# Kernel tuning notes

Hardware: AMD Instinct MI355X
Metric: run time of the kernel (lower is better)

The kernel has to match this reference:

```python
import jax, jax.numpy as jnp
import numpy as np

D_MODEL = 1024
N_HEADS = 16
HEAD_DIM = D_MODEL // N_HEADS


def setup_inputs() -> dict:
    key = jax.random.key(0)
    k0, k1, k2, k3, k4, k5 = jax.random.split(key, 6)
    s = 1.0 / np.sqrt(D_MODEL)
    return {
        "q": jax.random.normal(k0, (2, 2048, D_MODEL), dtype=jnp.float32),
        "Wq": jax.random.normal(k1, (D_MODEL, D_MODEL), dtype=jnp.float32) * s,
        "Wk": jax.random.normal(k2, (D_MODEL, D_MODEL), dtype=jnp.float32) * s,
        "Wv": jax.random.normal(k3, (D_MODEL, D_MODEL), dtype=jnp.float32) * s,
        "Wo": jax.random.normal(k4, (D_MODEL, D_MODEL), dtype=jnp.float32) * s,
        "bo": jax.random.normal(k5, (D_MODEL,), dtype=jnp.float32) * 0.01,
    }


def _split_heads(x):
    b, s, _ = x.shape
    return x.reshape(b, s, N_HEADS, HEAD_DIM).transpose(0, 2, 1, 3)  # [b,h,s,d]


def reference(q, Wq, Wk, Wv, Wo, bo):
    # self-attention: k = v = q
    qh = _split_heads(q @ Wq)  # [b,h,s,d]
    kh = _split_heads(q @ Wk)
    vh = _split_heads(q @ Wv)
    scale = 1.0 / np.sqrt(HEAD_DIM).astype(np.float32)
    scores = jnp.einsum("bhqd,bhkd->bhqk", qh, kh) * scale
    attn = jax.nn.softmax(scores, axis=-1)
    ctx = jnp.einsum("bhqk,bhkd->bhqd", attn, vh)
    b, h, s, d = ctx.shape
    ctx = ctx.transpose(0, 2, 1, 3).reshape(b, s, h * d)
    return ctx @ Wo + bo
```

## Files before the change

kernel.cpp:

```cpp
#include <hip/hip_runtime.h>
#include <cstdint>

typedef unsigned short u16;
typedef __bf16 bf16x8 __attribute__((ext_vector_type(8)));
typedef __bf16 bf16x2 __attribute__((ext_vector_type(2)));
typedef float floatx4 __attribute__((ext_vector_type(4)));
typedef unsigned short u16x4 __attribute__((ext_vector_type(4)));
typedef unsigned short u16x8 __attribute__((ext_vector_type(8)));

#define MFMA16(a, b, c) __builtin_amdgcn_mfma_f32_16x16x32_bf16((a), (b), (c), 0, 0, 0)
#define QSCALE_LOG2E 0.18033688011112042f


typedef __attribute__((address_space(3))) void as3_void;
typedef __attribute__((address_space(1))) void as1_void;

static __device__ __forceinline__ void async_load16(const void* g, void* l) {
  __builtin_amdgcn_global_load_lds((as1_void*)(uintptr_t)g, (as3_void*)(uintptr_t)l,
                                   16, 0, 0);
}

static __device__ __forceinline__ u16 f2bf(float f) {
  union { float f; unsigned int u; } v; v.f = f;
  unsigned int u = v.u;
  u += 0x7fffu + ((u >> 16) & 1u);
  return (u16)(u >> 16);
}

static __device__ __forceinline__ u16x4 pack_bf4(float a, float b, float c, float d) {
#if __has_builtin(__builtin_amdgcn_cvt_pk_bf16_f32)
  union { u16x4 v4; bf16x2 v2[2]; } u;
  u.v2[0] = __builtin_amdgcn_cvt_pk_bf16_f32(a, b);
  u.v2[1] = __builtin_amdgcn_cvt_pk_bf16_f32(c, d);
  return u.v4;
#else
  u16x4 r; r[0] = f2bf(a); r[1] = f2bf(b); r[2] = f2bf(c); r[3] = f2bf(d);
  return r;
#endif
}

static __device__ __forceinline__ unsigned pack_bf2(float a, float b) {
#if __has_builtin(__builtin_amdgcn_cvt_pk_bf16_f32)
  union { bf16x2 v; unsigned u; } x;
  x.v = __builtin_amdgcn_cvt_pk_bf16_f32(a, b);
  return x.u;
#else
  return (unsigned)f2bf(a) | ((unsigned)f2bf(b) << 16);
#endif
}

static __device__ __forceinline__ float fast_exp2(float x) {
#if __has_builtin(__builtin_amdgcn_exp2f)
  return __builtin_amdgcn_exp2f(x);
#else
  return exp2f(x);
#endif
}


__global__ __launch_bounds__(256) void prep_kernel(
    const float* __restrict__ w0, const float* __restrict__ w1,
    const float* __restrict__ w2, const float* __restrict__ w3,
    u16* __restrict__ wout,
    const float* __restrict__ xin, u16* __restrict__ xout) {
  if (blockIdx.z == 4) {
    int blk = blockIdx.y * 16 + blockIdx.x;
    size_t base = (size_t)blk * 16384 + (size_t)threadIdx.x * 8;
#pragma unroll
    for (int r = 0; r < 8; r++) {
      size_t i = base + (size_t)r * 2048;
      float4 a = *(const float4*)(xin + i);
      float4 b = *(const float4*)(xin + i + 4);
      u16x8 o;
      o[0] = f2bf(a.x); o[1] = f2bf(a.y); o[2] = f2bf(a.z); o[3] = f2bf(a.w);
      o[4] = f2bf(b.x); o[5] = f2bf(b.y); o[6] = f2bf(b.z); o[7] = f2bf(b.w);
      *(u16x8*)(xout + i) = o;
    }
    return;
  }
  __shared__ u16 t[64][65];
  const float* in = (blockIdx.z == 0) ? w0 : (blockIdx.z == 1) ? w1
                    : (blockIdx.z == 2) ? w2 : w3;
  u16* oz = wout + (size_t)blockIdx.z * (1024 * 1024);
  const int tid = threadIdx.x;
  const int x = tid & 63, y0 = tid >> 6;
  const int bx = blockIdx.x * 64, by = blockIdx.y * 64;
#pragma unroll
  for (int p = 0; p < 16; p++) {
    int y = y0 + p * 4;
    t[y][x] = f2bf(in[(size_t)(by + y) * 1024 + bx + x]);
  }
  __syncthreads();
#pragma unroll
  for (int p = 0; p < 16; p++) {
    int r = y0 + p * 4;
    oz[(size_t)(bx + r) * 1024 + by + x] = t[x][r];
  }
}


__global__ __launch_bounds__(256, 3) void gemm_qkv_kernel(
    const u16* __restrict__ A, const u16* __restrict__ BT,
    u16* __restrict__ out, u16* __restrict__ outVT) {
  __shared__ u16 As[128 * 32];
  __shared__ u16 Bs[128 * 32];
  __shared__ u16 tb[64 * 136];
  const int tid = threadIdx.x;
  const int w = tid >> 6, lane = tid & 63;
  const int bm = blockIdx.y * 128, bn = blockIdx.x * 128;
  const int z = blockIdx.z;
  const int K = 1024, N = 1024;
  const u16* Bz = BT + (size_t)z * N * K;

  const int c0 = w * 2, c1 = c0 + 1;
  const int mA0 = c0 * 16 + (lane >> 2), mA1 = c1 * 16 + (lane >> 2);
  const int kg0 = (lane & 3) ^ ((mA0 >> 1) & 3);
  const int kg1 = (lane & 3) ^ ((mA1 >> 1) & 3);
  const u16* agp0 = A + (size_t)(bm + mA0) * K + kg0 * 8;
  const u16* agp1 = A + (size_t)(bm + mA1) * K + kg1 * 8;
  const u16* bgp0 = Bz + (size_t)(bn + mA0) * K + kg0 * 8;
  const u16* bgp1 = Bz + (size_t)(bn + mA1) * K + kg1 * 8;
  u16* ald0 = As + c0 * 512; u16* ald1 = As + c1 * 512;
  u16* bld0 = Bs + c0 * 512; u16* bld1 = Bs + c1 * 512;

  const int wm = (w >> 1) * 64, wn = (w & 1) * 64;
  floatx4 acc[4][4] = {};

  int a_off[4], b_off[4];
#pragma unroll
  for (int i = 0; i < 4; i++) {
    int m = wm + i * 16 + (lane & 15);
    a_off[i] = m * 32 + (((lane >> 4) ^ ((m >> 1) & 3)) * 8);
    int n = wn + i * 16 + (lane & 15);
    b_off[i] = n * 32 + (((lane >> 4) ^ ((n >> 1) & 3)) * 8);
  }

  for (int k0 = 0; k0 < K; k0 += 32) {
    __syncthreads();
    async_load16(agp0 + k0, ald0);
    async_load16(agp1 + k0, ald1);
    async_load16(bgp0 + k0, bld0);
    async_load16(bgp1 + k0, bld1);
    __syncthreads();
    bf16x8 af[4], bf[4];
#pragma unroll
    for (int i = 0; i < 4; i++) af[i] = *(const bf16x8*)(As + a_off[i]);
#pragma unroll
    for (int j = 0; j < 4; j++) bf[j] = *(const bf16x8*)(Bs + b_off[j]);
#pragma unroll
    for (int i = 0; i < 4; i++)
#pragma unroll
      for (int j = 0; j < 4; j++)
        acc[i][j] = MFMA16(af[i], bf[j], acc[i][j]);
  }

  const int roff = (lane >> 4) * 4;
  const int coff = lane & 15;
  if (z == 2) {
    const int b = bm >> 11, s0 = bm & 2047;
#pragma unroll
    for (int half = 0; half < 2; half++) {
      __syncthreads();
      if ((w & 1) == half) {
#pragma unroll
        for (int i = 0; i < 4; i++) {
          int s_local = wm + i * 16 + roff;
#pragma unroll
          for (int j = 0; j < 4; j++) {
            int c_local = j * 16 + coff;
            u16x4 pk = pack_bf4(acc[i][j][0], acc[i][j][1],
                                acc[i][j][2], acc[i][j][3]);
            *(u16x4*)(tb + c_local * 136 + s_local) = pk;
          }
        }
      }
      __syncthreads();
#pragma unroll
      for (int p = 0; p < 4; p++) {
        int c_local = (tid >> 4) & 15;
        int row = p * 16 + c_local;
        int so = tid & 15;
        int cg = bn + half * 64 + row;
        int h = cg >> 6, d = cg & 63;
        u16x8 vv = *(const u16x8*)(tb + row * 136 + so * 8);
        *(u16x8*)(outVT + ((size_t)(b * 16 + h) * 64 + d) * 2048 + s0 + so * 8) = vv;
      }
    }
  } else {
    const float sc = (z == 0) ? QSCALE_LOG2E : 1.0f;
    u16* outz = out + (size_t)z * 4096 * 1024;
#pragma unroll
    for (int i = 0; i < 4; i++) {
      int r0 = bm + wm + i * 16 + roff;
#pragma unroll
      for (int j = 0; j < 4; j++) {
        int c = bn + wn + j * 16 + coff;
#pragma unroll
        for (int r = 0; r < 4; r++)
          outz[(size_t)(r0 + r) * N + c] = f2bf(acc[i][j][r] * sc);
      }
    }
  }
}


__global__ __launch_bounds__(256, 2) void gemm_o_kernel(
    const u16* __restrict__ A, const u16* __restrict__ BT,
    const float* __restrict__ bias, float* __restrict__ out) {
  __shared__ u16 As[128 * 32];
  __shared__ u16 Bs[64 * 32];
  const int tid = threadIdx.x;
  const int w = tid >> 6, lane = tid & 63;
  const int bm = blockIdx.y * 128, bn = blockIdx.x * 64;
  const int K = 1024, N = 1024;

  const u16* gp[3]; u16* ld[3];
#pragma unroll
  for (int i = 0; i < 3; i++) {
    int c = w * 3 + i;
    if (c < 8) {
      int m = c * 16 + (lane >> 2);
      int kg = (lane & 3) ^ ((m >> 1) & 3);
      gp[i] = A + (size_t)(bm + m) * K + kg * 8;
      ld[i] = As + c * 512;
    } else {
      int cb = c - 8;
      int n = cb * 16 + (lane >> 2);
      int kg = (lane & 3) ^ ((n >> 1) & 3);
      gp[i] = BT + (size_t)(bn + n) * K + kg * 8;
      ld[i] = Bs + cb * 512;
    }
  }

  const int wm = (w >> 1) * 64, wn = (w & 1) * 32;
  floatx4 acc[4][2] = {};

  int a_off[4], b_off[2];
#pragma unroll
  for (int i = 0; i < 4; i++) {
    int m = wm + i * 16 + (lane & 15);
    a_off[i] = m * 32 + (((lane >> 4) ^ ((m >> 1) & 3)) * 8);
  }
#pragma unroll
  for (int j = 0; j < 2; j++) {
    int n = wn + j * 16 + (lane & 15);
    b_off[j] = n * 32 + (((lane >> 4) ^ ((n >> 1) & 3)) * 8);
  }

  for (int k0 = 0; k0 < K; k0 += 32) {
    __syncthreads();
    async_load16(gp[0] + k0, ld[0]);
    async_load16(gp[1] + k0, ld[1]);
    async_load16(gp[2] + k0, ld[2]);
    __syncthreads();
    bf16x8 af[4], bf[2];
#pragma unroll
    for (int i = 0; i < 4; i++) af[i] = *(const bf16x8*)(As + a_off[i]);
#pragma unroll
    for (int j = 0; j < 2; j++) bf[j] = *(const bf16x8*)(Bs + b_off[j]);
#pragma unroll
    for (int i = 0; i < 4; i++)
#pragma unroll
      for (int j = 0; j < 2; j++)
        acc[i][j] = MFMA16(af[i], bf[j], acc[i][j]);
  }

  const int roff = (lane >> 4) * 4;
  const int coff = lane & 15;
#pragma unroll
  for (int i = 0; i < 4; i++) {
    int r0 = bm + wm + i * 16 + roff;
#pragma unroll
    for (int j = 0; j < 2; j++) {
      int c = bn + wn + j * 16 + coff;
      float bv = bias[c];
#pragma unroll
      for (int r = 0; r < 4; r++)
        out[(size_t)(r0 + r) * N + c] = acc[i][j][r] + bv;
    }
  }
}


__global__ __launch_bounds__(512, 4) void attn_kernel(
    const u16* __restrict__ Q, const u16* __restrict__ Kx,
    const u16* __restrict__ VT, u16* __restrict__ ctx) {
  __shared__ __align__(16) u16 lds[32768];
  const int tid = threadIdx.x;
  const int w = tid >> 6, lane = tid & 63;
  const int qq = w >> 1, sh = w & 1;
  const int quad = lane >> 4;
  const int bid = blockIdx.x;
  const int bh = (bid >> 7) * 8 + (bid & 7);
  const int q0 = ((bid >> 3) & 15) * 128;
  const int b = bh >> 4, h = bh & 15;
  const u16* Qh = Q + (size_t)b * 2048 * 1024 + h * 64;
  const u16* Kh = Kx + (size_t)b * 2048 * 1024 + h * 64;
  const u16* Vh = VT + (size_t)bh * 64 * 2048;

  const u16* kgp[2]; const u16* vgp[2];
  int kc[2], vc[2];
#pragma unroll
  for (int i = 0; i < 2; i++) {
    int c = w * 2 + i;
    int sl = c * 8 + (lane >> 3);
    int dg = (lane & 7) ^ (lane >> 3);
    kgp[i] = Kh + (size_t)sl * 1024 + dg * 8;
    kc[i] = c * 512;
    int dl = c * 4 + quad;
    int sg = (lane & 15) ^ (dl & 15);
    vgp[i] = Vh + (size_t)dl * 2048 + sg * 8;
    vc[i] = 8192 + c * 512;
  }

  auto issue_tile = [&](int buf, int t) {
    u16* dst = lds + buf * 16384;
    const size_t k0 = (size_t)t * 128;
#pragma unroll
    for (int i = 0; i < 2; i++) {
      async_load16(kgp[i] + k0 * 1024, dst + kc[i]);
      async_load16(vgp[i] + k0, dst + vc[i]);
    }
  };

  issue_tile(0, 0);

  const int qbase = q0 + qq * 32;
  bf16x8 qf[2][2];
#pragma unroll
  for (int qt = 0; qt < 2; qt++)
#pragma unroll
    for (int ks = 0; ks < 2; ks++)
      qf[qt][ks] = *(const bf16x8*)(Qh + (size_t)(qbase + qt * 16 + (lane & 15)) * 1024 +
                                    ks * 32 + quad * 8);

  bf16x8 onesf;
#pragma unroll
  for (int i = 0; i < 8; i++) onesf[i] = (__bf16)1.0f;
  const floatx4 zero4 = {};

  const int slot_k0 = quad ^ (lane & 7);
  const int slot_k1 = (4 + quad) ^ (lane & 7);
  const int koff0 = sh * 4096 + (lane & 15) * 64 + slot_k0 * 8;
  const int koff1 = sh * 4096 + (lane & 15) * 64 + slot_k1 * 8;
  const int sq = ((quad & 1) << 1) | (quad >> 1);

  floatx4 o[2][4] = {};
  floatx4 lacc[2] = {};

  asm volatile("s_waitcnt vmcnt(0)" ::: "memory");

#pragma unroll 2
  for (int t = 0; t < 16; ++t) {
    __builtin_amdgcn_s_barrier();
    __builtin_amdgcn_sched_barrier(0);
    if (t < 15) issue_tile((t + 1) & 1, t + 1);
    const u16* Ksb = lds + (t & 1) * 16384;
    const u16* Vsb = Ksb + 8192;

    floatx4 st[4][2];
#pragma unroll
    for (int si = 0; si < 4; si++) {
      bf16x8 kf0 = *(const bf16x8*)(Ksb + koff0 + si * 1024);
      bf16x8 kf1 = *(const bf16x8*)(Ksb + koff1 + si * 1024);
#pragma unroll
      for (int qt = 0; qt < 2; qt++)
        st[si][qt] = MFMA16(kf1, qf[qt][1], MFMA16(kf0, qf[qt][0], zero4));
    }

    unsigned pa[2][4], pb[2][4];
#pragma unroll
    for (int si = 0; si < 4; si++)
#pragma unroll
      for (int qt = 0; qt < 2; qt++) {
        pa[qt][si] = pack_bf2(fast_exp2(st[si][qt][0]), fast_exp2(st[si][qt][1]));
        pb[qt][si] = pack_bf2(fast_exp2(st[si][qt][2]), fast_exp2(st[si][qt][3]));
      }

    bf16x8 pf[2][2];
#pragma unroll
    for (int qt = 0; qt < 2; qt++)
#pragma unroll
      for (int ksl = 0; ksl < 2; ksl++) {
        unsigned x0 = pa[qt][2 * ksl], x1 = pa[qt][2 * ksl + 1];
        unsigned y0 = pb[qt][2 * ksl], y1 = pb[qt][2 * ksl + 1];
        asm("v_permlane16_swap_b32 %0, %1" : "+v"(x0), "+v"(x1));
        asm("v_permlane16_swap_b32 %0, %1" : "+v"(y0), "+v"(y1));
        union { unsigned u[4]; bf16x8 v; } uu;
        uu.u[0] = x0; uu.u[1] = y0; uu.u[2] = x1; uu.u[3] = y1;
        pf[qt][ksl] = uu.v;
      }

#pragma unroll
    for (int ksl = 0; ksl < 2; ksl++) {
      int kb = sh * 2 + ksl;
      bf16x8 vf[4];
#pragma unroll
      for (int jt = 0; jt < 4; jt++) {
        int d = jt * 16 + (lane & 15);
        int slot = (kb * 4 + sq) ^ (d & 15);
        vf[jt] = *(const bf16x8*)(Vsb + d * 128 + slot * 8);
      }
#pragma unroll
      for (int qt = 0; qt < 2; qt++) {
#pragma unroll
        for (int jt = 0; jt < 4; jt++)
          o[qt][jt] = MFMA16(pf[qt][ksl], vf[jt], o[qt][jt]);
        lacc[qt] = MFMA16(pf[qt][ksl], onesf, lacc[qt]);
      }
    }
    asm volatile("s_waitcnt vmcnt(0)" ::: "memory");
  }

  __syncthreads();
  floatx4* dump  = (floatx4*)lds;
  floatx4* ldump = (floatx4*)(lds + 16384);
  if (sh == 1) {
    int base = qq * 512;
#pragma unroll
    for (int qt = 0; qt < 2; qt++)
#pragma unroll
      for (int jt = 0; jt < 4; jt++)
        dump[base + (qt * 4 + jt) * 64 + lane] = o[qt][jt];
#pragma unroll
    for (int qt = 0; qt < 2; qt++)
      ldump[qq * 128 + qt * 64 + lane] = lacc[qt];
  }
  __syncthreads();
  if (sh == 0) {
    int base = qq * 512;
#pragma unroll
    for (int qt = 0; qt < 2; qt++)
#pragma unroll
      for (int jt = 0; jt < 4; jt++)
        o[qt][jt] += dump[base + (qt * 4 + jt) * 64 + lane];
#pragma unroll
    for (int qt = 0; qt < 2; qt++)
      lacc[qt] += ldump[qq * 128 + qt * 64 + lane];
#pragma unroll
    for (int qt = 0; qt < 2; qt++)
#pragma unroll
      for (int r = 0; r < 4; r++) {
        float inv = 1.0f / lacc[qt][r];
        int s = qbase + qt * 16 + quad * 4 + r;
#pragma unroll
        for (int j = 0; j < 4; j++) {
          int c = h * 64 + j * 16 + (lane & 15);
          ctx[(size_t)(b * 2048 + s) * 1024 + c] = f2bf(o[qt][j][r] * inv);
        }
      }
  }
}


extern "C" void kernel_launch(void* const* d_in, const int* in_sizes, int n_in,
                              void* d_out, int out_size, void* d_ws, size_t ws_size,
                              hipStream_t stream) {
  (void)in_sizes; (void)n_in; (void)out_size; (void)ws_size;
  const float* x  = (const float*)d_in[0];
  const float* Wq = (const float*)d_in[1];
  const float* Wk = (const float*)d_in[2];
  const float* Wv = (const float*)d_in[3];
  const float* Wo = (const float*)d_in[4];
  const float* bo = (const float*)d_in[5];
  u16* ws = (u16*)d_ws;
  const size_t MM = 1024 * 1024;
  u16* WT  = ws;
  u16* WoT = ws + 3 * MM;
  u16* Xb  = ws + 4 * MM;
  u16* QKV = ws + 8 * MM;
  u16* VTp = ws + 20 * MM;
  u16* CTX = ws + 24 * MM;

  dim3 blk(256);
  prep_kernel<<<dim3(16, 16, 5), blk, 0, stream>>>(Wq, Wk, Wv, Wo, WT, x, Xb);
  gemm_qkv_kernel<<<dim3(8, 32, 3), blk, 0, stream>>>(Xb, WT, QKV, VTp);
  attn_kernel<<<dim3(512, 1, 1), dim3(512), 0, stream>>>(QKV, QKV + 4 * MM, VTp, CTX);
  gemm_o_kernel<<<dim3(16, 32, 1), blk, 0, stream>>>(CTX, WoT, bo, (float*)d_out);
}
```

Measured before the change: 182.6 us.

## Double-buffer GEMM k-loops and software-pipeline PV against QK in attention

Both projection GEMMs now use two LDS buffers: the next k-tile's async global-to-LDS load is issued before computing the current one, and each iteration needs one barrier instead of two. This is meant to hide global load latency behind the MFMA work. In the attention kernel, the P·V MFMAs for the previous tile now run after the Q·K MFMAs of the current tile, with the V fragments loaded before the barrier, and a final epilogue handles the last tile. The unused V buffer is zeroed at the start so the first zero-probability PV step cannot pick up NaNs. The cost is more LDS per block and more registers held live, which could reduce occupancy.

```diff
diff --git a/kernel.cpp b/kernel.cpp
--- a/kernel.cpp
+++ b/kernel.cpp
@@ -102,8 +102,8 @@
 __global__ __launch_bounds__(256, 3) void gemm_qkv_kernel(
     const u16* __restrict__ A, const u16* __restrict__ BT,
     u16* __restrict__ out, u16* __restrict__ outVT) {
-  __shared__ u16 As[128 * 32];
-  __shared__ u16 Bs[128 * 32];
+  __shared__ u16 As[2 * 4096];
+  __shared__ u16 Bs[2 * 4096];
   __shared__ u16 tb[64 * 136];
   const int tid = threadIdx.x;
   const int w = tid >> 6, lane = tid & 63;
@@ -120,8 +120,6 @@
   const u16* agp1 = A + (size_t)(bm + mA1) * K + kg1 * 8;
   const u16* bgp0 = Bz + (size_t)(bn + mA0) * K + kg0 * 8;
   const u16* bgp1 = Bz + (size_t)(bn + mA1) * K + kg1 * 8;
-  u16* ald0 = As + c0 * 512; u16* ald1 = As + c1 * 512;
-  u16* bld0 = Bs + c0 * 512; u16* bld1 = Bs + c1 * 512;
 
   const int wm = (w >> 1) * 64, wn = (w & 1) * 64;
   floatx4 acc[4][4] = {};
@@ -135,23 +133,36 @@
     b_off[i] = n * 32 + (((lane >> 4) ^ ((n >> 1) & 3)) * 8);
   }
 
-  for (int k0 = 0; k0 < K; k0 += 32) {
-    __syncthreads();
-    async_load16(agp0 + k0, ald0);
-    async_load16(agp1 + k0, ald1);
-    async_load16(bgp0 + k0, bld0);
-    async_load16(bgp1 + k0, bld1);
-    __syncthreads();
+  auto issueQ = [&](int buf, int k0) {
+    u16* ab = As + buf * 4096;
+    u16* bb = Bs + buf * 4096;
+    async_load16(agp0 + k0, ab + c0 * 512);
+    async_load16(agp1 + k0, ab + c1 * 512);
+    async_load16(bgp0 + k0, bb + c0 * 512);
+    async_load16(bgp1 + k0, bb + c1 * 512);
+  };
+
+  issueQ(0, 0);
+  asm volatile("s_waitcnt vmcnt(0)" ::: "memory");
+  __builtin_amdgcn_s_barrier();
+
+#pragma unroll 2
+  for (int kk = 0; kk < 32; ++kk) {
+    if (kk < 31) issueQ((kk + 1) & 1, (kk + 1) * 32);
+    const u16* Ab = As + (kk & 1) * 4096;
+    const u16* Bb = Bs + (kk & 1) * 4096;
     bf16x8 af[4], bf[4];
 #pragma unroll
-    for (int i = 0; i < 4; i++) af[i] = *(const bf16x8*)(As + a_off[i]);
-#pragma unroll
-    for (int j = 0; j < 4; j++) bf[j] = *(const bf16x8*)(Bs + b_off[j]);
+    for (int i = 0; i < 4; i++) af[i] = *(const bf16x8*)(Ab + a_off[i]);
+#pragma unroll
+    for (int j = 0; j < 4; j++) bf[j] = *(const bf16x8*)(Bb + b_off[j]);
 #pragma unroll
     for (int i = 0; i < 4; i++)
 #pragma unroll
       for (int j = 0; j < 4; j++)
         acc[i][j] = MFMA16(af[i], bf[j], acc[i][j]);
+    asm volatile("s_waitcnt vmcnt(0) lgkmcnt(0)" ::: "memory");
+    __builtin_amdgcn_s_barrier();
   }
 
   const int roff = (lane >> 4) * 4;
@@ -207,14 +218,15 @@
 __global__ __launch_bounds__(256, 2) void gemm_o_kernel(
     const u16* __restrict__ A, const u16* __restrict__ BT,
     const float* __restrict__ bias, float* __restrict__ out) {
-  __shared__ u16 As[128 * 32];
-  __shared__ u16 Bs[64 * 32];
+  __shared__ u16 As[2 * 4096];
+  __shared__ u16 Bs[2 * 2048];
   const int tid = threadIdx.x;
   const int w = tid >> 6, lane = tid & 63;
   const int bm = blockIdx.y * 128, bn = blockIdx.x * 64;
   const int K = 1024, N = 1024;
 
-  const u16* gp[3]; u16* ld[3];
+  const u16* gp[3];
+  u16* ldp[2][3];
 #pragma unroll
   for (int i = 0; i < 3; i++) {
     int c = w * 3 + i;
@@ -222,13 +234,15 @@
       int m = c * 16 + (lane >> 2);
       int kg = (lane & 3) ^ ((m >> 1) & 3);
       gp[i] = A + (size_t)(bm + m) * K + kg * 8;
-      ld[i] = As + c * 512;
+      ldp[0][i] = As + c * 512;
+      ldp[1][i] = As + 4096 + c * 512;
     } else {
       int cb = c - 8;
       int n = cb * 16 + (lane >> 2);
       int kg = (lane & 3) ^ ((n >> 1) & 3);
       gp[i] = BT + (size_t)(bn + n) * K + kg * 8;
-      ld[i] = Bs + cb * 512;
+      ldp[0][i] = Bs + cb * 512;
+      ldp[1][i] = Bs + 2048 + cb * 512;
     }
   }
 
@@ -247,22 +261,33 @@
     b_off[j] = n * 32 + (((lane >> 4) ^ ((n >> 1) & 3)) * 8);
   }
 
-  for (int k0 = 0; k0 < K; k0 += 32) {
-    __syncthreads();
-    async_load16(gp[0] + k0, ld[0]);
-    async_load16(gp[1] + k0, ld[1]);
-    async_load16(gp[2] + k0, ld[2]);
-    __syncthreads();
+  auto issueO = [&](int buf, int k0) {
+#pragma unroll
+    for (int i = 0; i < 3; i++)
+      async_load16(gp[i] + k0, buf ? ldp[1][i] : ldp[0][i]);
+  };
+
+  issueO(0, 0);
+  asm volatile("s_waitcnt vmcnt(0)" ::: "memory");
+  __builtin_amdgcn_s_barrier();
+
+#pragma unroll 2
+  for (int kk = 0; kk < 32; ++kk) {
+    if (kk < 31) issueO((kk + 1) & 1, (kk + 1) * 32);
+    const u16* Ab = As + (kk & 1) * 4096;
+    const u16* Bb = Bs + (kk & 1) * 2048;
     bf16x8 af[4], bf[2];
 #pragma unroll
-    for (int i = 0; i < 4; i++) af[i] = *(const bf16x8*)(As + a_off[i]);
-#pragma unroll
-    for (int j = 0; j < 2; j++) bf[j] = *(const bf16x8*)(Bs + b_off[j]);
+    for (int i = 0; i < 4; i++) af[i] = *(const bf16x8*)(Ab + a_off[i]);
+#pragma unroll
+    for (int j = 0; j < 2; j++) bf[j] = *(const bf16x8*)(Bb + b_off[j]);
 #pragma unroll
     for (int i = 0; i < 4; i++)
 #pragma unroll
       for (int j = 0; j < 2; j++)
         acc[i][j] = MFMA16(af[i], bf[j], acc[i][j]);
+    asm volatile("s_waitcnt vmcnt(0) lgkmcnt(0)" ::: "memory");
+    __builtin_amdgcn_s_barrier();
   }
 
   const int roff = (lane >> 4) * 4;
@@ -298,6 +323,12 @@
   const u16* Kh = Kx + (size_t)b * 2048 * 1024 + h * 64;
   const u16* Vh = VT + (size_t)bh * 64 * 2048;
 
+  {
+    u16x8 z8 = {};
+    *(u16x8*)(lds + 24576 + tid * 8) = z8;
+    *(u16x8*)(lds + 24576 + 4096 + tid * 8) = z8;
+  }
+
   const u16* kgp[2]; const u16* vgp[2];
   int kc[2], vc[2];
 #pragma unroll
@@ -344,19 +375,43 @@
   const int koff0 = sh * 4096 + (lane & 15) * 64 + slot_k0 * 8;
   const int koff1 = sh * 4096 + (lane & 15) * 64 + slot_k1 * 8;
   const int sq = ((quad & 1) << 1) | (quad >> 1);
+  int vf_off[2][4];
+#pragma unroll
+  for (int ksl = 0; ksl < 2; ksl++)
+#pragma unroll
+    for (int jt = 0; jt < 4; jt++) {
+      int d = jt * 16 + (lane & 15);
+      int kb = sh * 2 + ksl;
+      int slot = (kb * 4 + sq) ^ (d & 15);
+      vf_off[ksl][jt] = d * 128 + slot * 8;
+    }
 
   floatx4 o[2][4] = {};
   floatx4 lacc[2] = {};
+  bf16x8 pf_prev[2][2];
+#pragma unroll
+  for (int a = 0; a < 2; a++)
+#pragma unroll
+    for (int c = 0; c < 2; c++) pf_prev[a][c] = bf16x8{};
 
   asm volatile("s_waitcnt vmcnt(0)" ::: "memory");
+  __builtin_amdgcn_s_barrier();
 
 #pragma unroll 2
   for (int t = 0; t < 16; ++t) {
+    const u16* Ksb = lds + (t & 1) * 16384;
+    const u16* Vsb_prev = lds + ((t + 1) & 1) * 16384 + 8192;
+
+    bf16x8 vf[2][4];
+#pragma unroll
+    for (int ksl = 0; ksl < 2; ksl++)
+#pragma unroll
+      for (int jt = 0; jt < 4; jt++)
+        vf[ksl][jt] = *(const bf16x8*)(Vsb_prev + vf_off[ksl][jt]);
+    asm volatile("s_waitcnt lgkmcnt(0)" ::: "memory");
+    __builtin_amdgcn_sched_barrier(0);
     __builtin_amdgcn_s_barrier();
-    __builtin_amdgcn_sched_barrier(0);
     if (t < 15) issue_tile((t + 1) & 1, t + 1);
-    const u16* Ksb = lds + (t & 1) * 16384;
-    const u16* Vsb = Ksb + 8192;
 
     floatx4 st[4][2];
 #pragma unroll
@@ -368,6 +423,16 @@
         st[si][qt] = MFMA16(kf1, qf[qt][1], MFMA16(kf0, qf[qt][0], zero4));
     }
 
+#pragma unroll
+    for (int ksl = 0; ksl < 2; ksl++)
+#pragma unroll
+      for (int qt = 0; qt < 2; qt++) {
+#pragma unroll
+        for (int jt = 0; jt < 4; jt++)
+          o[qt][jt] = MFMA16(pf_prev[qt][ksl], vf[ksl][jt], o[qt][jt]);
+        lacc[qt] = MFMA16(pf_prev[qt][ksl], onesf, lacc[qt]);
+      }
+
     unsigned pa[2][4], pb[2][4];
 #pragma unroll
     for (int si = 0; si < 4; si++)
@@ -377,7 +442,6 @@
         pb[qt][si] = pack_bf2(fast_exp2(st[si][qt][2]), fast_exp2(st[si][qt][3]));
       }
 
-    bf16x8 pf[2][2];
 #pragma unroll
     for (int qt = 0; qt < 2; qt++)
 #pragma unroll
@@ -388,28 +452,30 @@
         asm("v_permlane16_swap_b32 %0, %1" : "+v"(y0), "+v"(y1));
         union { unsigned u[4]; bf16x8 v; } uu;
         uu.u[0] = x0; uu.u[1] = y0; uu.u[2] = x1; uu.u[3] = y1;
-        pf[qt][ksl] = uu.v;
-      }
-
-#pragma unroll
-    for (int ksl = 0; ksl < 2; ksl++) {
-      int kb = sh * 2 + ksl;
-      bf16x8 vf[4];
-#pragma unroll
-      for (int jt = 0; jt < 4; jt++) {
-        int d = jt * 16 + (lane & 15);
-        int slot = (kb * 4 + sq) ^ (d & 15);
-        vf[jt] = *(const bf16x8*)(Vsb + d * 128 + slot * 8);
-      }
+        pf_prev[qt][ksl] = uu.v;
+      }
+
+    asm volatile("s_waitcnt vmcnt(0)" ::: "memory");
+    __builtin_amdgcn_s_barrier();
+  }
+
+  {
+    const u16* Vsb = lds + 16384 + 8192;
+    bf16x8 vf[2][4];
+#pragma unroll
+    for (int ksl = 0; ksl < 2; ksl++)
+#pragma unroll
+      for (int jt = 0; jt < 4; jt++)
+        vf[ksl][jt] = *(const bf16x8*)(Vsb + vf_off[ksl][jt]);
+#pragma unroll
+    for (int ksl = 0; ksl < 2; ksl++)
 #pragma unroll
       for (int qt = 0; qt < 2; qt++) {
 #pragma unroll
         for (int jt = 0; jt < 4; jt++)
-          o[qt][jt] = MFMA16(pf[qt][ksl], vf[jt], o[qt][jt]);
-        lacc[qt] = MFMA16(pf[qt][ksl], onesf, lacc[qt]);
-      }
-    }
-    asm volatile("s_waitcnt vmcnt(0)" ::: "memory");
+          o[qt][jt] = MFMA16(pf_prev[qt][ksl], vf[ksl][jt], o[qt][jt]);
+        lacc[qt] = MFMA16(pf_prev[qt][ksl], onesf, lacc[qt]);
+      }
   }
 
   __syncthreads();
```

New measurement: 340.8 us. +86.6%, slower.
